# Kernel tuning notes

Hardware: AMD Instinct MI355X
Metric: run time of the kernel (lower is better)

## Reference

```python
import jax, jax.numpy as jnp
import numpy as np

_INV_SQRT2 = np.float32(0.7071067811865476)


def _dwt_last(u):
    """Single-level Haar DWT along the last axis (pywt 'haar' convention).
    cA[i] = (u[2i]+u[2i+1])/sqrt(2), cD[i] = (u[2i]-u[2i+1])/sqrt(2)."""
    e = u[..., 0::2]
    o = u[..., 1::2]
    return (e + o) * _INV_SQRT2, (e - o) * _INV_SQRT2


def _dwt2(x):
    """Single-level 2D Haar DWT over the last two axes, matching pywt.dwt2.
    Returns (cA, cH, cV, cD) = ('aa', 'da', 'ad', 'dd') where the first
    letter is the filter applied along axis -2 and the second along axis -1."""
    a1, d1 = _dwt_last(x)                      # filter along axis -1
    a1t, d1t = a1.swapaxes(-1, -2), d1.swapaxes(-1, -2)
    aa, da = _dwt_last(a1t)                    # filter along axis -2
    ad, dd = _dwt_last(d1t)
    return (aa.swapaxes(-1, -2), da.swapaxes(-1, -2),
            ad.swapaxes(-1, -2), dd.swapaxes(-1, -2))


def setup_inputs() -> dict:
    key = jax.random.key(0)
    B, C, H, W = 32, 3, 512, 512
    x = jax.random.normal(key, (B, C, H, W), dtype=jnp.float32)
    return {"x": x}


def reference(x):
    # pywt.wavedec2(x, 'haar', level=2) -> [cA2, (cH2,cV2,cD2), (cH1,cV1,cD1)]
    a1, h1, v1, d1 = _dwt2(x)    # level 1: [B,C,H/2,W/2]
    a2, h2, v2, d2 = _dwt2(a1)   # level 2: [B,C,H/4,W/4]
    return (a2, h2, v2, d2, h1, v1, d1)
```

## Files before the change

### kernel.cpp

```cpp
#include <hip/hip_runtime.h>


#define KINV 0.7071067811865476f

typedef float v4f __attribute__((ext_vector_type(4)));
typedef float v2f __attribute__((ext_vector_type(2)));

__global__ __launch_bounds__(256) void haar2_fused_kernel(
    const float* __restrict__ x, float* __restrict__ out, int nimg)
{
    const int tid = blockIdx.x * blockDim.x + threadIdx.x;
    const int c2  = tid & 127;
    const int r2  = (tid >> 7) & 127;
    const int img = tid >> 14;

    const int row0 = r2 * 4;
    const int col0 = c2 * 4;

    const size_t n2 = (size_t)nimg * 128 * 128;
    const size_t n1 = (size_t)nimg * 256 * 256;
    float* a2o = out;
    float* h2o = out + n2;
    float* v2o = out + 2 * n2;
    float* d2o = out + 3 * n2;
    float* h1o = out + 4 * n2;
    float* v1o = h1o + n1;
    float* d1o = h1o + 2 * n1;

    const size_t in_base = (size_t)img * (512 * 512) + (size_t)row0 * 512 + col0;
    v4f b[4];
    #pragma unroll
    for (int k = 0; k < 4; ++k)
        b[k] = *reinterpret_cast<const v4f*>(x + in_base + (size_t)k * 512);

    float p[4][4];
    #pragma unroll
    for (int k = 0; k < 4; ++k) {
        p[k][0] = b[k].x; p[k][1] = b[k].y;
        p[k][2] = b[k].z; p[k][3] = b[k].w;
    }

    float aa[2][2], da[2][2], ad[2][2], dd[2][2];
    #pragma unroll
    for (int i = 0; i < 2; ++i) {
        #pragma unroll
        for (int j = 0; j < 2; ++j) {
            const float p00 = p[2*i    ][2*j], p01 = p[2*i    ][2*j+1];
            const float p10 = p[2*i + 1][2*j], p11 = p[2*i + 1][2*j+1];
            const float sA = (p00 + p01) * KINV;
            const float sB = (p10 + p11) * KINV;
            const float dA = (p00 - p01) * KINV;
            const float dB = (p10 - p11) * KINV;
            aa[i][j] = (sA + sB) * KINV;
            da[i][j] = (sA - sB) * KINV;
            ad[i][j] = (dA + dB) * KINV;
            dd[i][j] = (dA - dB) * KINV;
        }
    }

    const size_t img1 = (size_t)img * 256 * 256;
    #pragma unroll
    for (int i = 0; i < 2; ++i) {
        const size_t off = img1 + (size_t)(2 * r2 + i) * 256 + 2 * c2;
        *reinterpret_cast<v2f*>(h1o + off) = (v2f){da[i][0], da[i][1]};
        *reinterpret_cast<v2f*>(v1o + off) = (v2f){ad[i][0], ad[i][1]};
        *reinterpret_cast<v2f*>(d1o + off) = (v2f){dd[i][0], dd[i][1]};
    }

    const float s0 = (aa[0][0] + aa[0][1]) * KINV;
    const float d0 = (aa[0][0] - aa[0][1]) * KINV;
    const float s1 = (aa[1][0] + aa[1][1]) * KINV;
    const float d1 = (aa[1][0] - aa[1][1]) * KINV;
    const size_t off2 = (size_t)img * 128 * 128 + (size_t)r2 * 128 + c2;
    a2o[off2] = (s0 + s1) * KINV;
    h2o[off2] = (s0 - s1) * KINV;
    v2o[off2] = (d0 + d1) * KINV;
    d2o[off2] = (d0 - d1) * KINV;
}

extern "C" void kernel_launch(void* const* d_in, const int* in_sizes, int n_in,
                              void* d_out, int out_size, void* d_ws, size_t ws_size,
                              hipStream_t stream) {
    const float* x = (const float*)d_in[0];
    float* out = (float*)d_out;
    const int nimg = in_sizes[0] / (512 * 512);
    const int total_threads = nimg * 128 * 128;
    const int block = 256;
    const int grid = total_threads / block;
    haar2_fused_kernel<<<grid, block, 0, stream>>>(x, out, nimg);
}
```

Baseline: 174.7 us.

## Widen per-thread tile to 4x16 with 16-byte stores and nontemporal writes

Each thread now processes four adjacent 4x4 input tiles (a 4x16 strip), issuing 16 vector loads up front behind a scheduling barrier, then emitting all outputs as 16-byte vector stores instead of 8-byte and scalar stores. Output stores use nontemporal hints to avoid polluting cache, and launch bounds request 3 blocks per CU. This aims to raise memory-level parallelism and store efficiency of a bandwidth-bound kernel, at the cost of higher register use and four times fewer threads. Load coalescing changes since lanes now stride by 64 bytes per row chunk.

```diff
diff --git a/kernel.cpp b/kernel.cpp
--- a/kernel.cpp
+++ b/kernel.cpp
@@ -4,18 +4,14 @@
 #define KINV 0.7071067811865476f
 
 typedef float v4f __attribute__((ext_vector_type(4)));
-typedef float v2f __attribute__((ext_vector_type(2)));
 
-__global__ __launch_bounds__(256) void haar2_fused_kernel(
+__global__ __launch_bounds__(256, 3) void haar2_fused_kernel(
     const float* __restrict__ x, float* __restrict__ out, int nimg)
 {
     const int tid = blockIdx.x * blockDim.x + threadIdx.x;
-    const int c2  = tid & 127;
-    const int r2  = (tid >> 7) & 127;
-    const int img = tid >> 14;
-
-    const int row0 = r2 * 4;
-    const int col0 = c2 * 4;
+    const int cx  = tid & 31;
+    const int r2  = (tid >> 5) & 127;
+    const int img = tid >> 12;
 
     const size_t n2 = (size_t)nimg * 128 * 128;
     const size_t n1 = (size_t)nimg * 256 * 256;
@@ -27,55 +23,87 @@
     float* v1o = h1o + n1;
     float* d1o = h1o + 2 * n1;
 
-    const size_t in_base = (size_t)img * (512 * 512) + (size_t)row0 * 512 + col0;
-    v4f b[4];
+    const size_t in_base =
+        (size_t)img * (512 * 512) + (size_t)(r2 * 4) * 512 + (size_t)cx * 16;
+
+    v4f b[4][4];
     #pragma unroll
-    for (int k = 0; k < 4; ++k)
-        b[k] = *reinterpret_cast<const v4f*>(x + in_base + (size_t)k * 512);
+    for (int t = 0; t < 4; ++t)
+        #pragma unroll
+        for (int k = 0; k < 4; ++k)
+            b[t][k] = *reinterpret_cast<const v4f*>(
+                x + in_base + (size_t)k * 512 + (size_t)t * 4);
 
-    float p[4][4];
+    __builtin_amdgcn_sched_barrier(0);
+
+    float a2v[4], h2v[4], v2v[4], d2v[4];
+    float h1r[2][8], v1r[2][8], d1r[2][8];
+
     #pragma unroll
-    for (int k = 0; k < 4; ++k) {
-        p[k][0] = b[k].x; p[k][1] = b[k].y;
-        p[k][2] = b[k].z; p[k][3] = b[k].w;
-    }
-
-    float aa[2][2], da[2][2], ad[2][2], dd[2][2];
-    #pragma unroll
-    for (int i = 0; i < 2; ++i) {
+    for (int t = 0; t < 4; ++t) {
+        float aa[2][2];
         #pragma unroll
-        for (int j = 0; j < 2; ++j) {
-            const float p00 = p[2*i    ][2*j], p01 = p[2*i    ][2*j+1];
-            const float p10 = p[2*i + 1][2*j], p11 = p[2*i + 1][2*j+1];
-            const float sA = (p00 + p01) * KINV;
-            const float sB = (p10 + p11) * KINV;
-            const float dA = (p00 - p01) * KINV;
-            const float dB = (p10 - p11) * KINV;
-            aa[i][j] = (sA + sB) * KINV;
-            da[i][j] = (sA - sB) * KINV;
-            ad[i][j] = (dA + dB) * KINV;
-            dd[i][j] = (dA - dB) * KINV;
+        for (int i = 0; i < 2; ++i) {
+            const v4f top = b[t][2 * i];
+            const v4f bot = b[t][2 * i + 1];
+            {
+                const float sA = (top.x + top.y) * KINV;
+                const float sB = (bot.x + bot.y) * KINV;
+                const float dA = (top.x - top.y) * KINV;
+                const float dB = (bot.x - bot.y) * KINV;
+                aa[i][0]            = (sA + sB) * KINV;
+                h1r[i][2 * t]       = (sA - sB) * KINV;
+                v1r[i][2 * t]       = (dA + dB) * KINV;
+                d1r[i][2 * t]       = (dA - dB) * KINV;
+            }
+            {
+                const float sA = (top.z + top.w) * KINV;
+                const float sB = (bot.z + bot.w) * KINV;
+                const float dA = (top.z - top.w) * KINV;
+                const float dB = (bot.z - bot.w) * KINV;
+                aa[i][1]            = (sA + sB) * KINV;
+                h1r[i][2 * t + 1]   = (sA - sB) * KINV;
+                v1r[i][2 * t + 1]   = (dA + dB) * KINV;
+                d1r[i][2 * t + 1]   = (dA - dB) * KINV;
+            }
         }
+        const float s0 = (aa[0][0] + aa[0][1]) * KINV;
+        const float d0 = (aa[0][0] - aa[0][1]) * KINV;
+        const float s1 = (aa[1][0] + aa[1][1]) * KINV;
+        const float d1 = (aa[1][0] - aa[1][1]) * KINV;
+        a2v[t] = (s0 + s1) * KINV;
+        h2v[t] = (s0 - s1) * KINV;
+        v2v[t] = (d0 + d1) * KINV;
+        d2v[t] = (d0 - d1) * KINV;
     }
 
     const size_t img1 = (size_t)img * 256 * 256;
     #pragma unroll
     for (int i = 0; i < 2; ++i) {
-        const size_t off = img1 + (size_t)(2 * r2 + i) * 256 + 2 * c2;
-        *reinterpret_cast<v2f*>(h1o + off) = (v2f){da[i][0], da[i][1]};
-        *reinterpret_cast<v2f*>(v1o + off) = (v2f){ad[i][0], ad[i][1]};
-        *reinterpret_cast<v2f*>(d1o + off) = (v2f){dd[i][0], dd[i][1]};
+        const size_t off = img1 + (size_t)(2 * r2 + i) * 256 + (size_t)cx * 8;
+        #pragma unroll
+        for (int h = 0; h < 2; ++h) {
+            __builtin_nontemporal_store(
+                (v4f){h1r[i][4*h], h1r[i][4*h+1], h1r[i][4*h+2], h1r[i][4*h+3]},
+                reinterpret_cast<v4f*>(h1o + off + 4 * h));
+            __builtin_nontemporal_store(
+                (v4f){v1r[i][4*h], v1r[i][4*h+1], v1r[i][4*h+2], v1r[i][4*h+3]},
+                reinterpret_cast<v4f*>(v1o + off + 4 * h));
+            __builtin_nontemporal_store(
+                (v4f){d1r[i][4*h], d1r[i][4*h+1], d1r[i][4*h+2], d1r[i][4*h+3]},
+                reinterpret_cast<v4f*>(d1o + off + 4 * h));
+        }
     }
 
-    const float s0 = (aa[0][0] + aa[0][1]) * KINV;
-    const float d0 = (aa[0][0] - aa[0][1]) * KINV;
-    const float s1 = (aa[1][0] + aa[1][1]) * KINV;
-    const float d1 = (aa[1][0] - aa[1][1]) * KINV;
-    const size_t off2 = (size_t)img * 128 * 128 + (size_t)r2 * 128 + c2;
-    a2o[off2] = (s0 + s1) * KINV;
-    h2o[off2] = (s0 - s1) * KINV;
-    v2o[off2] = (d0 + d1) * KINV;
-    d2o[off2] = (d0 - d1) * KINV;
+    const size_t off2 = (size_t)img * 128 * 128 + (size_t)r2 * 128 + (size_t)cx * 4;
+    __builtin_nontemporal_store((v4f){a2v[0], a2v[1], a2v[2], a2v[3]},
+                                reinterpret_cast<v4f*>(a2o + off2));
+    __builtin_nontemporal_store((v4f){h2v[0], h2v[1], h2v[2], h2v[3]},
+                                reinterpret_cast<v4f*>(h2o + off2));
+    __builtin_nontemporal_store((v4f){v2v[0], v2v[1], v2v[2], v2v[3]},
+                                reinterpret_cast<v4f*>(v2o + off2));
+    __builtin_nontemporal_store((v4f){d2v[0], d2v[1], d2v[2], d2v[3]},
+                                reinterpret_cast<v4f*>(d2o + off2));
 }
 
 extern "C" void kernel_launch(void* const* d_in, const int* in_sizes, int n_in,
@@ -84,7 +112,7 @@
     const float* x = (const float*)d_in[0];
     float* out = (float*)d_out;
     const int nimg = in_sizes[0] / (512 * 512);
-    const int total_threads = nimg * 128 * 128;
+    const int total_threads = nimg * 128 * 32;
     const int block = 256;
     const int grid = total_threads / block;
     haar2_fused_kernel<<<grid, block, 0, stream>>>(x, out, nimg);
```

Result: slower. 210.8 us (+20.7%).
